# Kernel optimization log

Measured on AMD Instinct MI355X. Metric: run time of the kernel, lower is better.

## Reference

```python
import jax, jax.numpy as jnp
import numpy as np

# Static config (mirrors init_kwargs)
B, D, H, W, C = 2, 8, 128, 128, 96
HEADS, HEAD_DIM = 3, 32
WD, WH, WW = 2, 8, 8
SHIFT = (WD // 2, WH // 2, WW // 2)
NWIN = (D // WD) * (H // WH) * (W // WW)   # windows per batch element
N = WD * WH * WW                            # tokens per window
SCALE = HEAD_DIM ** -0.5
MLP = 384
INNER = HEADS * HEAD_DIM


def _rel_index():
    # 3D relative-position index into the (2wd-1)(2wh-1)(2ww-1) bias table
    coords = np.stack(np.meshgrid(np.arange(WD), np.arange(WH), np.arange(WW), indexing='ij'))
    coords = coords.reshape(3, -1)                      # [3, N]
    rel = coords[:, :, None] - coords[:, None, :]       # [3, N, N]
    rel[0] += WD - 1; rel[1] += WH - 1; rel[2] += WW - 1
    return rel[0] * (2 * WH - 1) * (2 * WW - 1) + rel[1] * (2 * WW - 1) + rel[2]


def _attn_mask():
    # Standard shifted-window region mask: tokens from different pre-shift regions
    # must not attend to each other.
    img = np.zeros((D, H, W), dtype=np.int32)
    cnt = 0
    for ds in (slice(0, -WD), slice(-WD, -SHIFT[0]), slice(-SHIFT[0], None)):
        for hs in (slice(0, -WH), slice(-WH, -SHIFT[1]), slice(-SHIFT[1], None)):
            for ws in (slice(0, -WW), slice(-WW, -SHIFT[2]), slice(-SHIFT[2], None)):
                img[ds, hs, ws] = cnt; cnt += 1
    win = img.reshape(D // WD, WD, H // WH, WH, W // WW, WW)
    win = win.transpose(0, 2, 4, 1, 3, 5).reshape(NWIN, N)
    diff = win[:, :, None] - win[:, None, :]
    return np.where(diff != 0, -1e9, 0.0).astype(np.float32)  # [NWIN, N, N]


REL_IDX = jnp.asarray(_rel_index())     # [N, N] int
ATTN_MASK = jnp.asarray(_attn_mask())   # [NWIN, N, N] float


def layer_norm(x, g, b):
    mu = x.mean(-1, keepdims=True)
    var = ((x - mu) ** 2).mean(-1, keepdims=True)
    return (x - mu) * jax.lax.rsqrt(var + 1e-5) * g + b


def window_partition(x, b):
    # [B,D,H,W,C] -> [B, NWIN, N, C]
    x = x.reshape(b, D // WD, WD, H // WH, WH, W // WW, WW, C)
    x = x.transpose(0, 1, 3, 5, 2, 4, 6, 7)
    return x.reshape(b, NWIN, N, C)


def window_reverse(x, b):
    x = x.reshape(b, D // WD, H // WH, W // WW, WD, WH, WW, C)
    x = x.transpose(0, 1, 4, 2, 5, 3, 6, 7)
    return x.reshape(b, D, H, W, C)


def _forward(x, gamma1, beta1, w_qkv, w_out, b_out, rel_bias,
             gamma2, beta2, w1, b1, w2, b2):
    b = x.shape[0]
    # --- shifted window attention (prenorm + residual) ---
    h = layer_norm(x, gamma1, beta1)
    h = jnp.roll(h, shift=(-SHIFT[0], -SHIFT[1], -SHIFT[2]), axis=(1, 2, 3))
    hw = window_partition(h, b)                         # [B, nW, N, C]
    qkv = hw @ w_qkv                                    # [B, nW, N, 3*INNER]
    q, k, v = jnp.split(qkv, 3, axis=-1)
    def split_heads(t):
        return t.reshape(b, NWIN, N, HEADS, HEAD_DIM).transpose(0, 1, 3, 2, 4)
    q, k, v = split_heads(q), split_heads(k), split_heads(v)  # [B,nW,h,N,d]
    attn = jnp.einsum('bwhid,bwhjd->bwhij', q, k) * SCALE     # [B,nW,h,N,N]
    attn = attn + rel_bias[REL_IDX].transpose(2, 0, 1)        # + [h,N,N]
    attn = attn + ATTN_MASK[None, :, None, :, :]              # + [nW,1,N,N]
    attn = jax.nn.softmax(attn, axis=-1)
    out = jnp.einsum('bwhij,bwhjd->bwhid', attn, v)
    out = out.transpose(0, 1, 3, 2, 4).reshape(b, NWIN, N, INNER)
    out = out @ w_out + b_out                                 # [B,nW,N,C]
    out = window_reverse(out, b)
    out = jnp.roll(out, shift=SHIFT, axis=(1, 2, 3))
    x = x + out
    # --- MLP (prenorm + residual) ---
    h2 = layer_norm(x, gamma2, beta2)
    h2 = jax.nn.gelu(h2 @ w1 + b1) @ w2 + b2
    return x + h2


def setup_inputs() -> dict:
    key = jax.random.key(0)
    ks = jax.random.split(key, 8)
    s = 0.02
    table = (2 * WD - 1) * (2 * WH - 1) * (2 * WW - 1)
    return {
        'x': jax.random.normal(ks[0], (B, D, H, W, C), jnp.float32),
        'gamma1': jnp.ones((C,), jnp.float32),
        'beta1': jnp.zeros((C,), jnp.float32),
        'w_qkv': jax.random.normal(ks[1], (C, 3 * INNER), jnp.float32) * s,
        'w_out': jax.random.normal(ks[2], (INNER, C), jnp.float32) * s,
        'b_out': jnp.zeros((C,), jnp.float32),
        'rel_bias': jax.random.normal(ks[3], (table, HEADS), jnp.float32) * s,
        'gamma2': jnp.ones((C,), jnp.float32),
        'beta2': jnp.zeros((C,), jnp.float32),
        'w1': jax.random.normal(ks[4], (C, MLP), jnp.float32) * s,
        'b1': jnp.zeros((MLP,), jnp.float32),
        'w2': jax.random.normal(ks[5], (MLP, C), jnp.float32) * s,
        'b2': jnp.zeros((C,), jnp.float32),
    }


def reference(x, gamma1, beta1, w_qkv, w_out, b_out, rel_bias,
              gamma2, beta2, w1, b1, w2, b2):
    return _forward(x, gamma1, beta1, w_qkv, w_out, b_out, rel_bias,
                    gamma2, beta2, w1, b1, w2, b2)
```

## Files before the change

### kernel.cpp

```cpp
#include <hip/hip_runtime.h>
#include <hip/hip_bf16.h>

typedef __bf16 bf16;
typedef bf16 bf16x8 __attribute__((ext_vector_type(8)));
typedef bf16 bf16x4 __attribute__((ext_vector_type(4)));
typedef float f32x4 __attribute__((ext_vector_type(4)));

#define MFMA16(a, b, c) __builtin_amdgcn_mfma_f32_16x16x32_bf16((a), (b), (c), 0, 0, 0)

constexpr float ATT_SCALE = 0.17677669529663687f;


__global__ __launch_bounds__(256) void setup_kernel(
    const float* __restrict__ w_qkv, const float* __restrict__ w_out,
    const float* __restrict__ w1, const float* __restrict__ w2,
    const float* __restrict__ rel_bias,
    bf16* __restrict__ wqkvT, bf16* __restrict__ woutT,
    bf16* __restrict__ w1T, bf16* __restrict__ w2T,
    float* __restrict__ biasf)
{
    const int i = blockIdx.x * 256 + threadIdx.x;
    if (i < 27648) {
        int o = i / 96, c = i % 96;
        wqkvT[i] = (bf16)w_qkv[c * 288 + o];
    }
    if (i < 9216) {
        int o = i / 96, c = i % 96;
        woutT[i] = (bf16)w_out[c * 96 + o];
    }
    if (i < 36864) {
        int o = i / 96, c = i % 96;
        w1T[i] = (bf16)w1[c * 384 + o];
    }
    if (i < 36864) {
        int o = i / 384, k = i % 384;
        w2T[i] = (bf16)w2[k * 96 + o];
    }
    if (i < 49152) {
        int h = i >> 14;
        int r = (i >> 7) & 127, cj = i & 127;
        int tdi = r >> 6, thi = (r >> 3) & 7, twi = r & 7;
        int tdj = cj >> 6, thj = (cj >> 3) & 7, twj = cj & 7;
        int relidx = (tdi - tdj + 1) * 225 + (thi - thj + 7) * 15 + (twi - twj + 7);
        biasf[i] = rel_bias[relidx * 3 + h];
    }
}

__global__ __launch_bounds__(512) void attn_kernel(
    const float* __restrict__ x,
    const float* __restrict__ gamma1, const float* __restrict__ beta1,
    const bf16* __restrict__ wqkvT, const bf16* __restrict__ woutT,
    const float* __restrict__ b_out, const float* __restrict__ biasf,
    float* __restrict__ xres)
{
    __shared__ bf16 hw[128][104];
    __shared__ bf16 qb[128][40];
    __shared__ bf16 kb[128][40];
    __shared__ bf16 vb[32][136];
    __shared__ bf16 pb[128][136];
    __shared__ bf16 ao[128][104];
    __shared__ int region[128];
    __shared__ int srcs[128];

    const int tid = threadIdx.x;
    const int lane = tid & 63;
    const int wave = tid >> 6;
    const int l15 = lane & 15;
    const int g = lane >> 4;

    const int blk = blockIdx.x;
    const int bb = blk >> 10;
    const int widx = blk & 1023;
    const int wd = widx >> 8, wh = (widx >> 4) & 15, ww = widx & 15;

    {
        const int n = tid >> 2;
        const int q4 = tid & 3;
        const int td = n >> 6, th = (n >> 3) & 7, tw = n & 7;
        const int d = wd * 2 + td, h = wh * 8 + th, w = ww * 8 + tw;
        const int d0 = (d + 1) & 7;
        const int h0 = (h + 4) & 127;
        const int w0 = (w + 4) & 127;
        const int tok = ((bb * 8 + d0) * 128 + h0) * 128 + w0;
        if (q4 == 0) {
            const int rd = d < 6 ? 0 : (d < 7 ? 1 : 2);
            const int rh = h < 120 ? 0 : (h < 124 ? 1 : 2);
            const int rw = w < 120 ? 0 : (w < 124 ? 1 : 2);
            region[n] = rd * 9 + rh * 3 + rw;
            srcs[n] = tok;
        }
        const float4* xp = reinterpret_cast<const float4*>(x + (size_t)tok * 96 + q4 * 24);
        float v[24];
        float s = 0.f, ss = 0.f;
        #pragma unroll
        for (int i = 0; i < 6; ++i) {
            float4 f = xp[i];
            v[4*i+0] = f.x; v[4*i+1] = f.y; v[4*i+2] = f.z; v[4*i+3] = f.w;
            s  += f.x + f.y + f.z + f.w;
            ss += f.x*f.x + f.y*f.y + f.z*f.z + f.w*f.w;
        }
        s  += __shfl_xor(s, 1);  ss += __shfl_xor(ss, 1);
        s  += __shfl_xor(s, 2);  ss += __shfl_xor(ss, 2);
        const float mu = s * (1.f / 96.f);
        const float rstd = rsqrtf(ss * (1.f / 96.f) - mu * mu + 1e-5f);
        #pragma unroll
        for (int i = 0; i < 24; ++i) {
            const int c = q4 * 24 + i;
            hw[n][c] = (bf16)((v[i] - mu) * rstd * gamma1[c] + beta1[c]);
        }
    }
    __syncthreads();

    const int arow = wave * 16 + l15;

    for (int head = 0; head < 3; ++head) {
        {
            bf16x8 afr[3];
            #pragma unroll
            for (int ks = 0; ks < 3; ++ks)
                afr[ks] = *reinterpret_cast<const bf16x8*>(&hw[arow][ks * 32 + g * 8]);
            #pragma unroll
            for (int ct = 0; ct < 6; ++ct) {
                const int part = ct >> 1;
                const int cc = (ct & 1) * 16 + l15;
                const int ocol = part * 96 + head * 32 + cc;
                f32x4 acc = {0.f, 0.f, 0.f, 0.f};
                #pragma unroll
                for (int ks = 0; ks < 3; ++ks) {
                    const bf16x8 bfr = *reinterpret_cast<const bf16x8*>(
                        &wqkvT[(size_t)ocol * 96 + ks * 32 + g * 8]);
                    acc = MFMA16(afr[ks], bfr, acc);
                }
                if (part == 0) {
                    #pragma unroll
                    for (int r = 0; r < 4; ++r) qb[wave * 16 + g * 4 + r][cc] = (bf16)acc[r];
                } else if (part == 1) {
                    #pragma unroll
                    for (int r = 0; r < 4; ++r) kb[wave * 16 + g * 4 + r][cc] = (bf16)acc[r];
                } else {
                    bf16x4 pk;
                    #pragma unroll
                    for (int r = 0; r < 4; ++r) pk[r] = (bf16)acc[r];
                    *reinterpret_cast<bf16x4*>(&vb[cc][wave * 16 + g * 4]) = pk;
                }
            }
        }
        __syncthreads();

        f32x4 sacc[8];
        {
            const bf16x8 qf = *reinterpret_cast<const bf16x8*>(&qb[arow][g * 8]);
            #pragma unroll
            for (int ct = 0; ct < 8; ++ct) {
                const bf16x8 kf = *reinterpret_cast<const bf16x8*>(&kb[ct * 16 + l15][g * 8]);
                f32x4 z = {0.f, 0.f, 0.f, 0.f};
                sacc[ct] = MFMA16(qf, kf, z);
            }
        }
        int regrow[4];
        #pragma unroll
        for (int r = 0; r < 4; ++r) regrow[r] = region[wave * 16 + g * 4 + r];
        int regcol[8];
        #pragma unroll
        for (int ct = 0; ct < 8; ++ct) regcol[ct] = region[ct * 16 + l15];
        const float* bh = biasf + head * 16384;
        #pragma unroll
        for (int ct = 0; ct < 8; ++ct) {
            const int scol = ct * 16 + l15;
            #pragma unroll
            for (int r = 0; r < 4; ++r) {
                const int srow = wave * 16 + g * 4 + r;
                float sv = sacc[ct][r] * ATT_SCALE + bh[srow * 128 + scol];
                sv += (regrow[r] == regcol[ct]) ? 0.f : -1e9f;
                sacc[ct][r] = sv;
            }
        }
        float mx[4], sum[4], rinv[4];
        #pragma unroll
        for (int r = 0; r < 4; ++r) {
            float m = sacc[0][r];
            #pragma unroll
            for (int ct = 1; ct < 8; ++ct) m = fmaxf(m, sacc[ct][r]);
            mx[r] = m;
        }
        #pragma unroll
        for (int w2 = 1; w2 < 16; w2 <<= 1) {
            #pragma unroll
            for (int r = 0; r < 4; ++r) mx[r] = fmaxf(mx[r], __shfl_xor(mx[r], w2));
        }
        #pragma unroll
        for (int r = 0; r < 4; ++r) sum[r] = 0.f;
        #pragma unroll
        for (int ct = 0; ct < 8; ++ct) {
            #pragma unroll
            for (int r = 0; r < 4; ++r) {
                float p = __expf(sacc[ct][r] - mx[r]);
                sacc[ct][r] = p;
                sum[r] += p;
            }
        }
        #pragma unroll
        for (int w2 = 1; w2 < 16; w2 <<= 1) {
            #pragma unroll
            for (int r = 0; r < 4; ++r) sum[r] += __shfl_xor(sum[r], w2);
        }
        #pragma unroll
        for (int r = 0; r < 4; ++r) rinv[r] = 1.f / sum[r];
        #pragma unroll
        for (int ct = 0; ct < 8; ++ct) {
            const int scol = ct * 16 + l15;
            #pragma unroll
            for (int r = 0; r < 4; ++r)
                pb[wave * 16 + g * 4 + r][scol] = (bf16)sacc[ct][r];
        }
        {
            bf16x8 pf[4];
            #pragma unroll
            for (int ks = 0; ks < 4; ++ks)
                pf[ks] = *reinterpret_cast<const bf16x8*>(&pb[arow][ks * 32 + g * 8]);
            #pragma unroll
            for (int ct = 0; ct < 2; ++ct) {
                f32x4 oacc = {0.f, 0.f, 0.f, 0.f};
                #pragma unroll
                for (int ks = 0; ks < 4; ++ks) {
                    const bf16x8 vf = *reinterpret_cast<const bf16x8*>(
                        &vb[ct * 16 + l15][ks * 32 + g * 8]);
                    oacc = MFMA16(pf[ks], vf, oacc);
                }
                #pragma unroll
                for (int r = 0; r < 4; ++r)
                    ao[wave * 16 + g * 4 + r][head * 32 + ct * 16 + l15] =
                        (bf16)(oacc[r] * rinv[r]);
            }
        }
        __syncthreads();
    }

    {
        bf16x8 af[3];
        #pragma unroll
        for (int ks = 0; ks < 3; ++ks)
            af[ks] = *reinterpret_cast<const bf16x8*>(&ao[arow][ks * 32 + g * 8]);
        int tsrc[4];
        #pragma unroll
        for (int r = 0; r < 4; ++r) tsrc[r] = srcs[wave * 16 + g * 4 + r];
        #pragma unroll
        for (int ct = 0; ct < 6; ++ct) {
            const int col = ct * 16 + l15;
            f32x4 acc = {0.f, 0.f, 0.f, 0.f};
            #pragma unroll
            for (int ks = 0; ks < 3; ++ks) {
                const bf16x8 bfr = *reinterpret_cast<const bf16x8*>(
                    &woutT[(size_t)col * 96 + ks * 32 + g * 8]);
                acc = MFMA16(af[ks], bfr, acc);
            }
            const float bo = b_out[col];
            #pragma unroll
            for (int r = 0; r < 4; ++r) {
                const size_t a = (size_t)tsrc[r] * 96 + col;
                xres[a] = x[a] + acc[r] + bo;
            }
        }
    }
}

__device__ __forceinline__ float gelu_tanh(float v) {
    const float a = 0.7978845608028654f * (v + 0.044715f * v * v * v);
    const float e = __expf(2.f * a);
    const float t = 1.f - 2.f / (e + 1.f);
    return 0.5f * v * (1.f + t);
}

__global__ __launch_bounds__(256) void mlp_kernel(
    float* __restrict__ xres,
    const float* __restrict__ gamma2, const float* __restrict__ beta2,
    const bf16* __restrict__ w1T, const float* __restrict__ b1,
    const bf16* __restrict__ w2T, const float* __restrict__ b2)
{
    __shared__ bf16 hw[64][104];
    __shared__ bf16 h1[64][392];

    const int tid = threadIdx.x;
    const int lane = tid & 63;
    const int wave = tid >> 6;
    const int l15 = lane & 15;
    const int g = lane >> 4;
    const size_t tok0 = (size_t)blockIdx.x * 64;

    {
        const int n = tid >> 2, q4 = tid & 3;
        const float4* xp = reinterpret_cast<const float4*>(xres + (tok0 + n) * 96 + q4 * 24);
        float v[24];
        float s = 0.f, ss = 0.f;
        #pragma unroll
        for (int i = 0; i < 6; ++i) {
            float4 f = xp[i];
            v[4*i+0] = f.x; v[4*i+1] = f.y; v[4*i+2] = f.z; v[4*i+3] = f.w;
            s  += f.x + f.y + f.z + f.w;
            ss += f.x*f.x + f.y*f.y + f.z*f.z + f.w*f.w;
        }
        s  += __shfl_xor(s, 1);  ss += __shfl_xor(ss, 1);
        s  += __shfl_xor(s, 2);  ss += __shfl_xor(ss, 2);
        const float mu = s * (1.f / 96.f);
        const float rstd = rsqrtf(ss * (1.f / 96.f) - mu * mu + 1e-5f);
        #pragma unroll
        for (int i = 0; i < 24; ++i) {
            const int c = q4 * 24 + i;
            hw[n][c] = (bf16)((v[i] - mu) * rstd * gamma2[c] + beta2[c]);
        }
    }
    __syncthreads();

    {
        #pragma unroll
        for (int rt = 0; rt < 4; ++rt) {
            bf16x8 af[3];
            #pragma unroll
            for (int ks = 0; ks < 3; ++ks)
                af[ks] = *reinterpret_cast<const bf16x8*>(&hw[rt * 16 + l15][ks * 32 + g * 8]);
            #pragma unroll
            for (int ct = 0; ct < 6; ++ct) {
                const int ocol = wave * 96 + ct * 16 + l15;
                f32x4 acc = {0.f, 0.f, 0.f, 0.f};
                #pragma unroll
                for (int ks = 0; ks < 3; ++ks) {
                    const bf16x8 bfr = *reinterpret_cast<const bf16x8*>(
                        &w1T[(size_t)ocol * 96 + ks * 32 + g * 8]);
                    acc = MFMA16(af[ks], bfr, acc);
                }
                const float bb1 = b1[ocol];
                #pragma unroll
                for (int r = 0; r < 4; ++r)
                    h1[rt * 16 + g * 4 + r][ocol] = (bf16)gelu_tanh(acc[r] + bb1);
            }
        }
    }
    __syncthreads();

    {
        const int arow = wave * 16 + l15;
        f32x4 acc[6];
        #pragma unroll
        for (int ct = 0; ct < 6; ++ct) { f32x4 z = {0.f,0.f,0.f,0.f}; acc[ct] = z; }
        #pragma unroll
        for (int ks = 0; ks < 12; ++ks) {
            const bf16x8 af = *reinterpret_cast<const bf16x8*>(&h1[arow][ks * 32 + g * 8]);
            #pragma unroll
            for (int ct = 0; ct < 6; ++ct) {
                const bf16x8 bfr = *reinterpret_cast<const bf16x8*>(
                    &w2T[(size_t)(ct * 16 + l15) * 384 + ks * 32 + g * 8]);
                acc[ct] = MFMA16(af, bfr, acc[ct]);
            }
        }
        #pragma unroll
        for (int ct = 0; ct < 6; ++ct) {
            const int col = ct * 16 + l15;
            const float bb2 = b2[col];
            #pragma unroll
            for (int r = 0; r < 4; ++r) {
                const size_t a = (tok0 + wave * 16 + g * 4 + r) * 96 + col;
                xres[a] = xres[a] + acc[ct][r] + bb2;
            }
        }
    }
}

extern "C" void kernel_launch(void* const* d_in, const int* in_sizes, int n_in,
                              void* d_out, int out_size, void* d_ws, size_t ws_size,
                              hipStream_t stream) {
    const float* x        = (const float*)d_in[0];
    const float* gamma1   = (const float*)d_in[1];
    const float* beta1    = (const float*)d_in[2];
    const float* w_qkv    = (const float*)d_in[3];
    const float* w_out    = (const float*)d_in[4];
    const float* b_out    = (const float*)d_in[5];
    const float* rel_bias = (const float*)d_in[6];
    const float* gamma2   = (const float*)d_in[7];
    const float* beta2    = (const float*)d_in[8];
    const float* w1       = (const float*)d_in[9];
    const float* b1       = (const float*)d_in[10];
    const float* w2       = (const float*)d_in[11];
    const float* b2       = (const float*)d_in[12];
    float* out = (float*)d_out;

    char* ws = (char*)d_ws;
    bf16*  wqkvT = (bf16*)(ws + 0);
    bf16*  woutT = (bf16*)(ws + 55296);
    bf16*  w1T   = (bf16*)(ws + 73728);
    bf16*  w2T   = (bf16*)(ws + 147456);
    float* biasf = (float*)(ws + 221184);

    setup_kernel<<<192, 256, 0, stream>>>(w_qkv, w_out, w1, w2, rel_bias,
                                          wqkvT, woutT, w1T, w2T, biasf);
    attn_kernel<<<2048, 512, 0, stream>>>(x, gamma1, beta1, wqkvT, woutT,
                                          b_out, biasf, out);
    mlp_kernel<<<4096, 256, 0, stream>>>(out, gamma2, beta2, w1T, b1, w2T, b2);
}
```

Baseline: 570.2 us.

## Keep attention probabilities and MLP hidden activations in registers via lane shuffles

The attention kernel now computes S transposed (K·Q) so each lane owns one query row. The P and attention-output fragments are repacked into MFMA operand layout with cross-lane shuffles, which removes the pb and ao shared buffers. The relative bias table is stored transposed to match the new access pattern, and launch bounds request higher occupancy. The MLP kernel becomes per-wave: it holds the 384-wide GELU activations packed in registers and shuffles them into A-fragments, which removes the h1 shared buffer and the block barriers, at the cost of heavier register pressure and more shuffle instructions.

```diff
diff --git a/kernel.cpp b/kernel.cpp
--- a/kernel.cpp
+++ b/kernel.cpp
@@ -1,14 +1,37 @@
 #include <hip/hip_runtime.h>
 #include <hip/hip_bf16.h>
+#include <stdint.h>
 
 typedef __bf16 bf16;
 typedef bf16 bf16x8 __attribute__((ext_vector_type(8)));
 typedef bf16 bf16x4 __attribute__((ext_vector_type(4)));
 typedef float f32x4 __attribute__((ext_vector_type(4)));
+typedef uint32_t u32;
 
 #define MFMA16(a, b, c) __builtin_amdgcn_mfma_f32_16x16x32_bf16((a), (b), (c), 0, 0, 0)
 
 constexpr float ATT_SCALE = 0.17677669529663687f;
+
+union FragU { u32 u[4]; bf16x8 v; };
+
+__device__ __forceinline__ u32 packbf(float lo, float hi) {
+    bf16 l = (bf16)lo, h = (bf16)hi;
+    unsigned short ls = __builtin_bit_cast(unsigned short, l);
+    unsigned short hs = __builtin_bit_cast(unsigned short, h);
+    return (u32)ls | ((u32)hs << 16);
+}
+
+__device__ __forceinline__ void quad_gather(FragU& f, u32 e01, u32 e23, u32 o01, u32 o23,
+                                            int srcA, int srcB, bool hi) {
+    u32 a0 = (u32)__shfl((int)e01, srcA), a1 = (u32)__shfl((int)e23, srcA);
+    u32 a2 = (u32)__shfl((int)o01, srcA), a3 = (u32)__shfl((int)o23, srcA);
+    u32 b0 = (u32)__shfl((int)e01, srcB), b1 = (u32)__shfl((int)e23, srcB);
+    u32 b2 = (u32)__shfl((int)o01, srcB), b3 = (u32)__shfl((int)o23, srcB);
+    f.u[0] = hi ? a2 : a0;
+    f.u[1] = hi ? a3 : a1;
+    f.u[2] = hi ? b2 : b0;
+    f.u[3] = hi ? b3 : b1;
+}
 
 
 __global__ __launch_bounds__(256) void setup_kernel(
@@ -17,7 +40,7 @@
     const float* __restrict__ rel_bias,
     bf16* __restrict__ wqkvT, bf16* __restrict__ woutT,
     bf16* __restrict__ w1T, bf16* __restrict__ w2T,
-    float* __restrict__ biasf)
+    float* __restrict__ biasfT)
 {
     const int i = blockIdx.x * 256 + threadIdx.x;
     if (i < 27648) {
@@ -42,23 +65,21 @@
         int tdi = r >> 6, thi = (r >> 3) & 7, twi = r & 7;
         int tdj = cj >> 6, thj = (cj >> 3) & 7, twj = cj & 7;
         int relidx = (tdi - tdj + 1) * 225 + (thi - thj + 7) * 15 + (twi - twj + 7);
-        biasf[i] = rel_bias[relidx * 3 + h];
-    }
-}
-
-__global__ __launch_bounds__(512) void attn_kernel(
+        biasfT[h * 16384 + cj * 128 + r] = rel_bias[relidx * 3 + h];
+    }
+}
+
+__global__ __launch_bounds__(512, 4) void attn_kernel(
     const float* __restrict__ x,
     const float* __restrict__ gamma1, const float* __restrict__ beta1,
     const bf16* __restrict__ wqkvT, const bf16* __restrict__ woutT,
-    const float* __restrict__ b_out, const float* __restrict__ biasf,
+    const float* __restrict__ b_out, const float* __restrict__ biasfT,
     float* __restrict__ xres)
 {
     __shared__ bf16 hw[128][104];
     __shared__ bf16 qb[128][40];
     __shared__ bf16 kb[128][40];
     __shared__ bf16 vb[32][136];
-    __shared__ bf16 pb[128][136];
-    __shared__ bf16 ao[128][104];
     __shared__ int region[128];
     __shared__ int srcs[128];
 
@@ -112,7 +133,14 @@
     __syncthreads();
 
     const int arow = wave * 16 + l15;
-
+    const int srcA = ((lane & 16) << 1) | (lane & 15);
+    const int srcB = srcA + 16;
+    const bool hi = (lane & 32) != 0;
+    const int qreg = region[arow];
+
+    FragU oa[3];
+
+    #pragma unroll
     for (int head = 0; head < 3; ++head) {
         {
             bf16x8 afr[3];
@@ -154,93 +182,75 @@
             for (int ct = 0; ct < 8; ++ct) {
                 const bf16x8 kf = *reinterpret_cast<const bf16x8*>(&kb[ct * 16 + l15][g * 8]);
                 f32x4 z = {0.f, 0.f, 0.f, 0.f};
-                sacc[ct] = MFMA16(qf, kf, z);
-            }
-        }
-        int regrow[4];
-        #pragma unroll
-        for (int r = 0; r < 4; ++r) regrow[r] = region[wave * 16 + g * 4 + r];
-        int regcol[8];
-        #pragma unroll
-        for (int ct = 0; ct < 8; ++ct) regcol[ct] = region[ct * 16 + l15];
-        const float* bh = biasf + head * 16384;
+                sacc[ct] = MFMA16(kf, qf, z);
+            }
+        }
+        {
+            const float* bh = biasfT + head * 16384;
+            #pragma unroll
+            for (int ct = 0; ct < 8; ++ct) {
+                #pragma unroll
+                for (int r = 0; r < 4; ++r) {
+                    const int k = ct * 16 + g * 4 + r;
+                    float sv = sacc[ct][r] * ATT_SCALE + bh[k * 128 + arow];
+                    sv += (region[k] == qreg) ? 0.f : -1e9f;
+                    sacc[ct][r] = sv;
+                }
+            }
+        }
+        float m = sacc[0][0];
+        #pragma unroll
+        for (int ct = 0; ct < 8; ++ct)
+            #pragma unroll
+            for (int r = 0; r < 4; ++r) m = fmaxf(m, sacc[ct][r]);
+        m = fmaxf(m, __shfl_xor(m, 16));
+        m = fmaxf(m, __shfl_xor(m, 32));
+        float sum = 0.f;
+        #pragma unroll
+        for (int ct = 0; ct < 8; ++ct)
+            #pragma unroll
+            for (int r = 0; r < 4; ++r) {
+                float p = __expf(sacc[ct][r] - m);
+                sacc[ct][r] = p;
+                sum += p;
+            }
+        sum += __shfl_xor(sum, 16);
+        sum += __shfl_xor(sum, 32);
+        const float rinv = 1.f / sum;
+
+        u32 P01[8], P23[8];
         #pragma unroll
         for (int ct = 0; ct < 8; ++ct) {
-            const int scol = ct * 16 + l15;
-            #pragma unroll
-            for (int r = 0; r < 4; ++r) {
-                const int srow = wave * 16 + g * 4 + r;
-                float sv = sacc[ct][r] * ATT_SCALE + bh[srow * 128 + scol];
-                sv += (regrow[r] == regcol[ct]) ? 0.f : -1e9f;
-                sacc[ct][r] = sv;
-            }
-        }
-        float mx[4], sum[4], rinv[4];
-        #pragma unroll
-        for (int r = 0; r < 4; ++r) {
-            float m = sacc[0][r];
-            #pragma unroll
-            for (int ct = 1; ct < 8; ++ct) m = fmaxf(m, sacc[ct][r]);
-            mx[r] = m;
-        }
-        #pragma unroll
-        for (int w2 = 1; w2 < 16; w2 <<= 1) {
-            #pragma unroll
-            for (int r = 0; r < 4; ++r) mx[r] = fmaxf(mx[r], __shfl_xor(mx[r], w2));
-        }
-        #pragma unroll
-        for (int r = 0; r < 4; ++r) sum[r] = 0.f;
-        #pragma unroll
-        for (int ct = 0; ct < 8; ++ct) {
-            #pragma unroll
-            for (int r = 0; r < 4; ++r) {
-                float p = __expf(sacc[ct][r] - mx[r]);
-                sacc[ct][r] = p;
-                sum[r] += p;
-            }
-        }
-        #pragma unroll
-        for (int w2 = 1; w2 < 16; w2 <<= 1) {
-            #pragma unroll
-            for (int r = 0; r < 4; ++r) sum[r] += __shfl_xor(sum[r], w2);
-        }
-        #pragma unroll
-        for (int r = 0; r < 4; ++r) rinv[r] = 1.f / sum[r];
-        #pragma unroll
-        for (int ct = 0; ct < 8; ++ct) {
-            const int scol = ct * 16 + l15;
-            #pragma unroll
-            for (int r = 0; r < 4; ++r)
-                pb[wave * 16 + g * 4 + r][scol] = (bf16)sacc[ct][r];
-        }
+            P01[ct] = packbf(sacc[ct][0], sacc[ct][1]);
+            P23[ct] = packbf(sacc[ct][2], sacc[ct][3]);
+        }
+        f32x4 acc2[2];
         {
-            bf16x8 pf[4];
-            #pragma unroll
-            for (int ks = 0; ks < 4; ++ks)
-                pf[ks] = *reinterpret_cast<const bf16x8*>(&pb[arow][ks * 32 + g * 8]);
-            #pragma unroll
-            for (int ct = 0; ct < 2; ++ct) {
-                f32x4 oacc = {0.f, 0.f, 0.f, 0.f};
-                #pragma unroll
-                for (int ks = 0; ks < 4; ++ks) {
-                    const bf16x8 vf = *reinterpret_cast<const bf16x8*>(
-                        &vb[ct * 16 + l15][ks * 32 + g * 8]);
-                    oacc = MFMA16(pf[ks], vf, oacc);
-                }
-                #pragma unroll
-                for (int r = 0; r < 4; ++r)
-                    ao[wave * 16 + g * 4 + r][head * 32 + ct * 16 + l15] =
-                        (bf16)(oacc[r] * rinv[r]);
-            }
+            f32x4 z = {0.f, 0.f, 0.f, 0.f};
+            acc2[0] = z; acc2[1] = z;
+        }
+        #pragma unroll
+        for (int ks = 0; ks < 4; ++ks) {
+            FragU pf;
+            quad_gather(pf, P01[2*ks], P23[2*ks], P01[2*ks+1], P23[2*ks+1], srcA, srcB, hi);
+            #pragma unroll
+            for (int dt = 0; dt < 2; ++dt) {
+                const bf16x8 vf = *reinterpret_cast<const bf16x8*>(
+                    &vb[dt * 16 + l15][ks * 32 + g * 8]);
+                acc2[dt] = MFMA16(vf, pf.v, acc2[dt]);
+            }
+        }
+        {
+            u32 E01 = packbf(acc2[0][0] * rinv, acc2[0][1] * rinv);
+            u32 E23 = packbf(acc2[0][2] * rinv, acc2[0][3] * rinv);
+            u32 O01 = packbf(acc2[1][0] * rinv, acc2[1][1] * rinv);
+            u32 O23 = packbf(acc2[1][2] * rinv, acc2[1][3] * rinv);
+            quad_gather(oa[head], E01, E23, O01, O23, srcA, srcB, hi);
         }
         __syncthreads();
     }
 
     {
-        bf16x8 af[3];
-        #pragma unroll
-        for (int ks = 0; ks < 3; ++ks)
-            af[ks] = *reinterpret_cast<const bf16x8*>(&ao[arow][ks * 32 + g * 8]);
         int tsrc[4];
         #pragma unroll
         for (int r = 0; r < 4; ++r) tsrc[r] = srcs[wave * 16 + g * 4 + r];
@@ -252,7 +262,7 @@
             for (int ks = 0; ks < 3; ++ks) {
                 const bf16x8 bfr = *reinterpret_cast<const bf16x8*>(
                     &woutT[(size_t)col * 96 + ks * 32 + g * 8]);
-                acc = MFMA16(af[ks], bfr, acc);
+                acc = MFMA16(oa[ks].v, bfr, acc);
             }
             const float bo = b_out[col];
             #pragma unroll
@@ -271,25 +281,24 @@
     return 0.5f * v * (1.f + t);
 }
 
-__global__ __launch_bounds__(256) void mlp_kernel(
+__global__ __launch_bounds__(256, 4) void mlp_kernel(
     float* __restrict__ xres,
     const float* __restrict__ gamma2, const float* __restrict__ beta2,
     const bf16* __restrict__ w1T, const float* __restrict__ b1,
     const bf16* __restrict__ w2T, const float* __restrict__ b2)
 {
-    __shared__ bf16 hw[64][104];
-    __shared__ bf16 h1[64][392];
+    __shared__ bf16 hw[4][16][104];
 
     const int tid = threadIdx.x;
     const int lane = tid & 63;
     const int wave = tid >> 6;
     const int l15 = lane & 15;
     const int g = lane >> 4;
-    const size_t tok0 = (size_t)blockIdx.x * 64;
+    const size_t trow = (size_t)blockIdx.x * 64 + wave * 16;
 
     {
-        const int n = tid >> 2, q4 = tid & 3;
-        const float4* xp = reinterpret_cast<const float4*>(xres + (tok0 + n) * 96 + q4 * 24);
+        const int n = lane >> 2, q4 = lane & 3;
+        const float4* xp = reinterpret_cast<const float4*>(xres + (trow + n) * 96 + q4 * 24);
         float v[24];
         float s = 0.f, ss = 0.f;
         #pragma unroll
@@ -306,61 +315,58 @@
         #pragma unroll
         for (int i = 0; i < 24; ++i) {
             const int c = q4 * 24 + i;
-            hw[n][c] = (bf16)((v[i] - mu) * rstd * gamma2[c] + beta2[c]);
-        }
-    }
-    __syncthreads();
-
-    {
-        #pragma unroll
-        for (int rt = 0; rt < 4; ++rt) {
-            bf16x8 af[3];
-            #pragma unroll
-            for (int ks = 0; ks < 3; ++ks)
-                af[ks] = *reinterpret_cast<const bf16x8*>(&hw[rt * 16 + l15][ks * 32 + g * 8]);
-            #pragma unroll
-            for (int ct = 0; ct < 6; ++ct) {
-                const int ocol = wave * 96 + ct * 16 + l15;
-                f32x4 acc = {0.f, 0.f, 0.f, 0.f};
-                #pragma unroll
-                for (int ks = 0; ks < 3; ++ks) {
-                    const bf16x8 bfr = *reinterpret_cast<const bf16x8*>(
-                        &w1T[(size_t)ocol * 96 + ks * 32 + g * 8]);
-                    acc = MFMA16(af[ks], bfr, acc);
-                }
-                const float bb1 = b1[ocol];
-                #pragma unroll
-                for (int r = 0; r < 4; ++r)
-                    h1[rt * 16 + g * 4 + r][ocol] = (bf16)gelu_tanh(acc[r] + bb1);
-            }
-        }
-    }
-    __syncthreads();
-
-    {
-        const int arow = wave * 16 + l15;
-        f32x4 acc[6];
-        #pragma unroll
-        for (int ct = 0; ct < 6; ++ct) { f32x4 z = {0.f,0.f,0.f,0.f}; acc[ct] = z; }
-        #pragma unroll
-        for (int ks = 0; ks < 12; ++ks) {
-            const bf16x8 af = *reinterpret_cast<const bf16x8*>(&h1[arow][ks * 32 + g * 8]);
-            #pragma unroll
-            for (int ct = 0; ct < 6; ++ct) {
-                const bf16x8 bfr = *reinterpret_cast<const bf16x8*>(
-                    &w2T[(size_t)(ct * 16 + l15) * 384 + ks * 32 + g * 8]);
-                acc[ct] = MFMA16(af, bfr, acc[ct]);
-            }
-        }
+            hw[wave][n][c] = (bf16)((v[i] - mu) * rstd * gamma2[c] + beta2[c]);
+        }
+    }
+
+    bf16x8 hfr[3];
+    #pragma unroll
+    for (int ks = 0; ks < 3; ++ks)
+        hfr[ks] = *reinterpret_cast<const bf16x8*>(&hw[wave][l15][ks * 32 + g * 8]);
+
+    u32 pk01[24], pk23[24];
+    #pragma unroll
+    for (int ot = 0; ot < 24; ++ot) {
+        const float4 b1v = *reinterpret_cast<const float4*>(b1 + ot * 16 + g * 4);
+        f32x4 acc = {0.f, 0.f, 0.f, 0.f};
+        #pragma unroll
+        for (int ks = 0; ks < 3; ++ks) {
+            const bf16x8 w1f = *reinterpret_cast<const bf16x8*>(
+                &w1T[(size_t)(ot * 16 + l15) * 96 + ks * 32 + g * 8]);
+            acc = MFMA16(w1f, hfr[ks], acc);
+        }
+        pk01[ot] = packbf(gelu_tanh(acc[0] + b1v.x), gelu_tanh(acc[1] + b1v.y));
+        pk23[ot] = packbf(gelu_tanh(acc[2] + b1v.z), gelu_tanh(acc[3] + b1v.w));
+    }
+
+    const int srcA = ((lane & 16) << 1) | (lane & 15);
+    const int srcB = srcA + 16;
+    const bool hi = (lane & 32) != 0;
+
+    f32x4 acc2[6];
+    #pragma unroll
+    for (int ct = 0; ct < 6; ++ct) { f32x4 z = {0.f,0.f,0.f,0.f}; acc2[ct] = z; }
+
+    #pragma unroll
+    for (int ks = 0; ks < 12; ++ks) {
+        FragU hf;
+        quad_gather(hf, pk01[2*ks], pk23[2*ks], pk01[2*ks+1], pk23[2*ks+1], srcA, srcB, hi);
         #pragma unroll
         for (int ct = 0; ct < 6; ++ct) {
-            const int col = ct * 16 + l15;
-            const float bb2 = b2[col];
-            #pragma unroll
-            for (int r = 0; r < 4; ++r) {
-                const size_t a = (tok0 + wave * 16 + g * 4 + r) * 96 + col;
-                xres[a] = xres[a] + acc[ct][r] + bb2;
-            }
+            const bf16x8 w2f = *reinterpret_cast<const bf16x8*>(
+                &w2T[(size_t)(ct * 16 + l15) * 384 + ks * 32 + g * 8]);
+            acc2[ct] = MFMA16(hf.v, w2f, acc2[ct]);
+        }
+    }
+
+    #pragma unroll
+    for (int ct = 0; ct < 6; ++ct) {
+        const int col = ct * 16 + l15;
+        const float bb2 = b2[col];
+        #pragma unroll
+        for (int r = 0; r < 4; ++r) {
+            const size_t a = (trow + g * 4 + r) * 96 + col;
+            xres[a] = xres[a] + acc2[ct][r] + bb2;
         }
     }
 }
@@ -384,15 +390,15 @@
     float* out = (float*)d_out;
 
     char* ws = (char*)d_ws;
-    bf16*  wqkvT = (bf16*)(ws + 0);
-    bf16*  woutT = (bf16*)(ws + 55296);
-    bf16*  w1T   = (bf16*)(ws + 73728);
-    bf16*  w2T   = (bf16*)(ws + 147456);
-    float* biasf = (float*)(ws + 221184);
+    bf16*  wqkvT  = (bf16*)(ws + 0);
+    bf16*  woutT  = (bf16*)(ws + 55296);
+    bf16*  w1T    = (bf16*)(ws + 73728);
+    bf16*  w2T    = (bf16*)(ws + 147456);
+    float* biasfT = (float*)(ws + 221184);
 
     setup_kernel<<<192, 256, 0, stream>>>(w_qkv, w_out, w1, w2, rel_bias,
-                                          wqkvT, woutT, w1T, w2T, biasf);
+                                          wqkvT, woutT, w1T, w2T, biasfT);
     attn_kernel<<<2048, 512, 0, stream>>>(x, gamma1, beta1, wqkvT, woutT,
-                                          b_out, biasf, out);
+                                          b_out, biasfT, out);
     mlp_kernel<<<4096, 256, 0, stream>>>(out, gamma2, beta2, w1T, b1, w2T, b2);
 }
```

Result: faster. 527.9 us (-7.4%).
